# Kernel tuning notes

Hardware: AMD Instinct MI355X
Metric: run time of the kernel (lower is better)

The kernel has to match this reference:

```python
import jax, jax.numpy as jnp
import numpy as np


def _degree_norms(src, dst, n_nodes):
    ones = jnp.ones(src.shape[0], dtype=jnp.float32)
    deg_out = jax.ops.segment_sum(ones, src, num_segments=n_nodes)
    deg_in = jax.ops.segment_sum(ones, dst, num_segments=n_nodes)
    # DGL GraphConv clamps degrees to min 1 before pow(-0.5)
    norm_src = jnp.power(jnp.maximum(deg_out, 1.0), -0.5)
    norm_dst = jnp.power(jnp.maximum(deg_in, 1.0), -0.5)
    return norm_src, norm_dst


def _graph_conv(h, src, dst, norm_src, norm_dst, W, b, activation):
    n_nodes = h.shape[0]
    # norm='both': scale source features, project, aggregate, scale dest
    x = h * norm_src[:, None]
    x = x @ W                                   # [N, out]
    m = x[src]                                  # gather  [E, out]
    agg = jax.ops.segment_sum(m, dst, num_segments=n_nodes)  # scatter-add [N, out]
    out = agg * norm_dst[:, None] + b
    if activation is not None:
        out = activation(out)
    return out


def setup_inputs() -> dict:
    key = jax.random.key(0)
    k = jax.random.split(key, 6)
    N, E, F, D = 100000, 1600000, 128, 128
    feature = jax.random.normal(k[0], (N, F), dtype=jnp.float32)
    src = jax.random.randint(k[1], (E,), 0, N, dtype=jnp.int32)
    dst = jax.random.randint(k[2], (E,), 0, N, dtype=jnp.int32)
    W1 = jax.random.normal(k[3], (F, D), dtype=jnp.float32) / np.sqrt(F)
    b1 = jnp.zeros((D,), dtype=jnp.float32)
    W2 = jax.random.normal(k[4], (D, D), dtype=jnp.float32) / np.sqrt(D)
    b2 = jnp.zeros((D,), dtype=jnp.float32)
    return {"feature": feature, "src": src, "dst": dst,
            "W1": W1, "b1": b1, "W2": W2, "b2": b2}


def reference(feature, src, dst, W1, b1, W2, b2):
    n_nodes = feature.shape[0]
    norm_src, norm_dst = _degree_norms(src, dst, n_nodes)
    # layer 0: relu; layer 1 (last): no activation
    h = _graph_conv(feature, src, dst, norm_src, norm_dst, W1, b1, jax.nn.relu)
    h = _graph_conv(h, src, dst, norm_src, norm_dst, W2, b2, None)
    return h
```

## Files before the change

kernel.cpp:

```cpp
#include <hip/hip_runtime.h>


#define RS_LOG 10
#define RS (1 << RS_LOG)

__device__ __forceinline__ unsigned pack_bf2(float a, float b) {
  unsigned ua = __float_as_uint(a);
  ua = ua + 0x7FFF + ((ua >> 16) & 1);
  unsigned ub = __float_as_uint(b);
  ub = ub + 0x7FFF + ((ub >> 16) & 1);
  return (ua >> 16) | (ub & 0xFFFF0000u);
}

__global__ void build_graph(const int* __restrict__ src, const int* __restrict__ dst,
                            int* __restrict__ cursor, int* __restrict__ deg_out,
                            int* __restrict__ padded, int E, int CAP) {
  int e = blockIdx.x * blockDim.x + threadIdx.x;
  if (e < E) {
    int s = src[e];
    int d = dst[e];
    atomicAdd(&deg_out[s], 1);
    int pos = atomicAdd(&cursor[d], 1);
    if (pos < CAP) padded[(size_t)d * CAP + pos] = s;
  }
}

__global__ __launch_bounds__(256) void partition_edges(
    const int* __restrict__ src, const int* __restrict__ dst, int* __restrict__ g_cnt,
    int* __restrict__ part_dst, unsigned short* __restrict__ part_src, int E, int NR, int CAPR,
    int EPB) {
  __shared__ int cntD[256], cntS[256], baseD[256], baseS[256];
  int t = threadIdx.x;
  int e0 = blockIdx.x * EPB;
  int e1 = min(e0 + EPB, E);
  for (int i = t; i < NR; i += 256) {
    cntD[i] = 0;
    cntS[i] = 0;
  }
  __syncthreads();
  for (int e = e0 + t; e < e1; e += 256) {
    atomicAdd(&cntD[dst[e] >> RS_LOG], 1);
    atomicAdd(&cntS[src[e] >> RS_LOG], 1);
  }
  __syncthreads();
  for (int i = t; i < NR; i += 256) {
    baseD[i] = atomicAdd(&g_cnt[i * 16], cntD[i]);
    baseS[i] = atomicAdd(&g_cnt[(NR + i) * 16], cntS[i]);
    cntD[i] = 0;
    cntS[i] = 0;
  }
  __syncthreads();
  for (int e = e0 + t; e < e1; e += 256) {
    int s = src[e];
    int d = dst[e];
    int rd = d >> RS_LOG;
    int rs = s >> RS_LOG;
    int pd = baseD[rd] + atomicAdd(&cntD[rd], 1);
    if (pd < CAPR) part_dst[(size_t)rd * CAPR + pd] = ((d & (RS - 1)) << 17) | s;
    int ps = baseS[rs] + atomicAdd(&cntS[rs], 1);
    if (ps < CAPR) part_src[(size_t)rs * CAPR + ps] = (unsigned short)(s & (RS - 1));
  }
}

__global__ __launch_bounds__(512) void build_structures(
    const int* __restrict__ g_cnt, const int* __restrict__ part_dst,
    const unsigned short* __restrict__ part_src, int* __restrict__ padded,
    int* __restrict__ deg_in, int* __restrict__ deg_out, int N, int NR, int CAPR, int CAP) {
  __shared__ int cur[RS];
  int t = threadIdx.x;
  int b = blockIdx.x;
  for (int i = t; i < RS; i += 512) cur[i] = 0;
  __syncthreads();
  if (b < NR) {
    int cnt = min(g_cnt[b * 16], CAPR);
    const int* p = part_dst + (size_t)b * CAPR;
    for (int i = t; i < cnt; i += 512) {
      int v = p[i];
      int dlow = v >> 17;
      int s = v & 0x1FFFF;
      int pos = atomicAdd(&cur[dlow], 1);
      if (pos < CAP) padded[((size_t)((b << RS_LOG) + dlow)) * CAP + pos] = s;
    }
    __syncthreads();
    int nbase = b << RS_LOG;
    for (int i = t; i < RS; i += 512) {
      int node = nbase + i;
      if (node < N) deg_in[node] = cur[i];
    }
  } else {
    int r = b - NR;
    int cnt = min(g_cnt[(NR + r) * 16], CAPR);
    const unsigned short* p = part_src + (size_t)r * CAPR;
    for (int i = t; i < cnt; i += 512) atomicAdd(&cur[p[i]], 1);
    __syncthreads();
    int nbase = r << RS_LOG;
    for (int i = t; i < RS; i += 512) {
      int node = nbase + i;
      if (node < N) deg_out[node] = cur[i];
    }
  }
}

__global__ void compute_norms(const int* __restrict__ deg_out, const int* __restrict__ deg_in,
                              float* __restrict__ norm_src, float* __restrict__ norm_dst, int N) {
  int i = blockIdx.x * blockDim.x + threadIdx.x;
  if (i < N) {
    norm_src[i] = rsqrtf((float)max(deg_out[i], 1));
    norm_dst[i] = rsqrtf((float)max(deg_in[i], 1));
  }
}

__global__ __launch_bounds__(512) void gemm_scale_bf(const float* __restrict__ X,
                                                     const float* __restrict__ W,
                                                     const float* __restrict__ norm,
                                                     unsigned* __restrict__ Ybf, int N) {
  __shared__ float Xl[64 * 129];
  int t = threadIdx.x;
  int r0 = blockIdx.x * 64;
  {
    const float4* X4 = (const float4*)(X + (size_t)r0 * 128);
#pragma unroll
    for (int j = 0; j < 4; j++) {
      int idx4 = t + j * 512;
      int r = idx4 >> 5;
      int c4 = idx4 & 31;
      float4 v = {0.f, 0.f, 0.f, 0.f};
      if (r0 + r < N) v = X4[idx4];
      float* dp = &Xl[r * 129 + c4 * 4];
      dp[0] = v.x;
      dp[1] = v.y;
      dp[2] = v.z;
      dp[3] = v.w;
    }
  }
  __syncthreads();
  int lane = t & 63;
  int wv = t >> 6;
  int c0 = __builtin_amdgcn_readfirstlane(wv * 16);
  float acc[16];
#pragma unroll
  for (int u = 0; u < 16; u++) acc[u] = 0.f;
  const float* xrow = &Xl[lane * 129];
#pragma unroll 4
  for (int k = 0; k < 128; k++) {
    float xk = xrow[k];
    const float* wp = W + k * 128 + c0;
#pragma unroll
    for (int u = 0; u < 16; u++) acc[u] = fmaf(wp[u], xk, acc[u]);
  }
  int r = r0 + lane;
  if (r < N) {
    float nn = norm[r];
    unsigned p[8];
#pragma unroll
    for (int q = 0; q < 8; q++) p[q] = pack_bf2(acc[2 * q] * nn, acc[2 * q + 1] * nn);
    uint4* yo = (uint4*)(Ybf + (size_t)r * 64 + (c0 >> 1));
    yo[0] = make_uint4(p[0], p[1], p[2], p[3]);
    yo[1] = make_uint4(p[4], p[5], p[6], p[7]);
  }
}

__global__ __launch_bounds__(256) void spmm_bf(const unsigned* __restrict__ Ybf,
                                               const int* __restrict__ padded,
                                               const int* __restrict__ deg_in,
                                               const float* __restrict__ norm_dst,
                                               const float* __restrict__ bias,
                                               float* __restrict__ out, int N, int CAP,
                                               int do_relu) {
  int t = threadIdx.x;
  int lane = t & 63;
  int wv = t >> 6;
  int v = blockIdx.x * 4 + wv;
  if (v >= N) return;
  int cnt = min(deg_in[v], CAP);
  int sidx = (lane < cnt) ? padded[(size_t)v * CAP + lane] : 0;
  float ax = 0.f, ay = 0.f;
  int i = 0;
  for (; i + 4 <= cnt; i += 4) {
    int s0 = __builtin_amdgcn_readlane(sidx, i);
    int s1 = __builtin_amdgcn_readlane(sidx, i + 1);
    int s2 = __builtin_amdgcn_readlane(sidx, i + 2);
    int s3 = __builtin_amdgcn_readlane(sidx, i + 3);
    unsigned w0 = Ybf[(size_t)s0 * 64 + lane];
    unsigned w1 = Ybf[(size_t)s1 * 64 + lane];
    unsigned w2 = Ybf[(size_t)s2 * 64 + lane];
    unsigned w3 = Ybf[(size_t)s3 * 64 + lane];
    ax += __uint_as_float(w0 << 16) + __uint_as_float(w1 << 16) +
          __uint_as_float(w2 << 16) + __uint_as_float(w3 << 16);
    ay += __uint_as_float(w0 & 0xFFFF0000u) + __uint_as_float(w1 & 0xFFFF0000u) +
          __uint_as_float(w2 & 0xFFFF0000u) + __uint_as_float(w3 & 0xFFFF0000u);
  }
  for (; i < cnt; i++) {
    int s = __builtin_amdgcn_readlane(sidx, i);
    unsigned w = Ybf[(size_t)s * 64 + lane];
    ax += __uint_as_float(w << 16);
    ay += __uint_as_float(w & 0xFFFF0000u);
  }
  float nd = norm_dst[v];
  float2 b = ((const float2*)bias)[lane];
  float2 r;
  r.x = ax * nd + b.x;
  r.y = ay * nd + b.y;
  if (do_relu) {
    r.x = fmaxf(r.x, 0.f);
    r.y = fmaxf(r.y, 0.f);
  }
  ((float2*)out)[(size_t)v * 64 + lane] = r;
}

extern "C" void kernel_launch(void* const* d_in, const int* in_sizes, int n_in,
                              void* d_out, int out_size, void* d_ws, size_t ws_size,
                              hipStream_t stream) {
  const float* feature = (const float*)d_in[0];
  const int* src = (const int*)d_in[1];
  const int* dst = (const int*)d_in[2];
  const float* W1 = (const float*)d_in[3];
  const float* b1 = (const float*)d_in[4];
  const float* W2 = (const float*)d_in[5];
  const float* b2 = (const float*)d_in[6];
  float* out = (float*)d_out;

  const int F = 128;
  int N = in_sizes[0] / F;
  int E = in_sizes[1];
  (void)n_in;
  (void)out_size;

  char* ws = (char*)d_ws;
  size_t off = 0;
  auto alloc = [&](size_t bytes) -> char* {
    char* p = ws + off;
    off = (off + bytes + 255) & ~(size_t)255;
    return p;
  };
  float* h_buf = (float*)alloc((size_t)N * F * 4);
  int* degs = (int*)alloc((size_t)2 * N * 4);
  int* deg_in_ = degs;
  int* deg_out_ = degs + N;
  float* norm_src = (float*)alloc((size_t)N * 4);
  float* norm_dst = (float*)alloc((size_t)N * 4);

  int NR = (N + RS - 1) >> RS_LOG;
  int CAPR = (E + NR - 1) / NR + 4096;
  CAPR = (CAPR + 31) & ~31;
  size_t part_bytes =
      (size_t)NR * CAPR * 4 + (size_t)NR * CAPR * 2 + (size_t)2 * NR * 16 * 4 + 1024;
  size_t avail = (ws_size > off) ? ws_size - off : 0;

  int CAP;
  bool partition_ok = (N <= 131072) && (NR <= 256);
  bool use_part;
  if (partition_ok && avail >= (size_t)N * 64 * 4 + part_bytes) {
    CAP = 64;
    use_part = true;
  } else if (partition_ok && avail >= (size_t)N * 48 * 4 + part_bytes) {
    CAP = 48;
    use_part = true;
  } else if (avail >= (size_t)N * 64 * 4 + (size_t)N * 4 + 256) {
    CAP = 64;
    use_part = false;
  } else if (avail >= (size_t)N * 48 * 4 + (size_t)N * 4 + 256) {
    CAP = 48;
    use_part = false;
  } else {
    CAP = 32;
    use_part = false;
  }
  int* padded = (int*)alloc((size_t)N * CAP * 4);

  if (use_part) {
    int* part_dst = (int*)alloc((size_t)NR * CAPR * 4);
    unsigned short* part_src = (unsigned short*)alloc((size_t)NR * CAPR * 2);
    int* g_cnt = (int*)alloc((size_t)2 * NR * 16 * 4);
    const int EPB = 4096;
    int NB = (E + EPB - 1) / EPB;
    hipMemsetAsync(g_cnt, 0, (size_t)2 * NR * 16 * 4, stream);
    partition_edges<<<NB, 256, 0, stream>>>(src, dst, g_cnt, part_dst, part_src, E, NR, CAPR,
                                            EPB);
    build_structures<<<2 * NR, 512, 0, stream>>>(g_cnt, part_dst, part_src, padded, deg_in_,
                                                 deg_out_, N, NR, CAPR, CAP);
  } else {
    int* cursor = (int*)alloc((size_t)N * 4);
    hipMemsetAsync(degs, 0, (size_t)2 * N * 4, stream);
    build_graph<<<(E + 255) / 256, 256, 0, stream>>>(src, dst, deg_in_, deg_out_, padded, E, CAP);
    (void)cursor;
  }
  compute_norms<<<(N + 255) / 256, 256, 0, stream>>>(deg_out_, deg_in_, norm_src, norm_dst, N);

  unsigned* ybf1 = (unsigned*)d_out;
  unsigned* ybf2;
  float* final_target;
  bool need_copy;
  size_t ybf_bytes = (size_t)N * 64 * 4;
  if (ws_size > off && ws_size - off >= ybf_bytes + 256) {
    ybf2 = (unsigned*)alloc(ybf_bytes);
    final_target = out;
    need_copy = false;
  } else {
    ybf2 = (unsigned*)d_out;
    final_target = h_buf;
    need_copy = true;
  }

  int gblocks = (N + 63) / 64;
  gemm_scale_bf<<<gblocks, 512, 0, stream>>>(feature, W1, norm_src, ybf1, N);
  spmm_bf<<<(N + 3) / 4, 256, 0, stream>>>(ybf1, padded, deg_in_, norm_dst, b1, h_buf, N, CAP, 1);
  gemm_scale_bf<<<gblocks, 512, 0, stream>>>(h_buf, W2, norm_src, ybf2, N);
  spmm_bf<<<(N + 3) / 4, 256, 0, stream>>>(ybf2, padded, deg_in_, norm_dst, b2, final_target, N,
                                           CAP, 0);
  if (need_copy) {
    hipMemcpyAsync(out, h_buf, (size_t)N * F * 4, hipMemcpyDeviceToDevice, stream);
  }
}
```

Measured before the change: 400.4 us.

## Replace FP32 FMA GEMM with split-bf16 MFMA GEMM using pre-transposed weights

Replaces the scalar FP32 dense projection with a matrix-core kernel using 16x16x32 bf16 MFMA. Activations and weights are split into high and low bf16 parts, and three MFMA products are summed to approximate FP32 accuracy. A new prep kernel converts and transposes each weight matrix once per call. The change targets compute time in the two GEMMs, at the cost of extra conversion ALU work and uncoalesced 2-byte output stores.

Measured after the change: 414.1 us. +3.4%, slower.

```diff
diff --git a/kernel.cpp b/kernel.cpp
--- a/kernel.cpp
+++ b/kernel.cpp
@@ -4,12 +4,12 @@
 #define RS_LOG 10
 #define RS (1 << RS_LOG)
 
-__device__ __forceinline__ unsigned pack_bf2(float a, float b) {
-  unsigned ua = __float_as_uint(a);
-  ua = ua + 0x7FFF + ((ua >> 16) & 1);
-  unsigned ub = __float_as_uint(b);
-  ub = ub + 0x7FFF + ((ub >> 16) & 1);
-  return (ua >> 16) | (ub & 0xFFFF0000u);
+typedef short bf16x8 __attribute__((ext_vector_type(8)));
+typedef float f32x4 __attribute__((ext_vector_type(4)));
+
+__device__ __forceinline__ unsigned short rne_bf16(float v) {
+  unsigned u = __float_as_uint(v);
+  return (unsigned short)((u + 0x7FFF + ((u >> 16) & 1)) >> 16);
 }
 
 __global__ void build_graph(const int* __restrict__ src, const int* __restrict__ dst,
@@ -110,53 +110,98 @@
   }
 }
 
-__global__ __launch_bounds__(512) void gemm_scale_bf(const float* __restrict__ X,
-                                                     const float* __restrict__ W,
-                                                     const float* __restrict__ norm,
-                                                     unsigned* __restrict__ Ybf, int N) {
-  __shared__ float Xl[64 * 129];
+__global__ __launch_bounds__(256) void prep_w(const float* __restrict__ W,
+                                              unsigned short* __restrict__ Wt_hi,
+                                              unsigned short* __restrict__ Wt_lo) {
+  int idx = blockIdx.x * 256 + threadIdx.x;
+  int k = idx >> 7;
+  int c = idx & 127;
+  float w = W[idx];
+  unsigned short h = rne_bf16(w);
+  float hf = __uint_as_float((unsigned)h << 16);
+  unsigned short l = rne_bf16(w - hf);
+  Wt_hi[c * 128 + k] = h;
+  Wt_lo[c * 128 + k] = l;
+}
+
+__global__ __launch_bounds__(256) void gemm_mfma(const float* __restrict__ X,
+                                                 const unsigned short* __restrict__ Wt_hi,
+                                                 const unsigned short* __restrict__ Wt_lo,
+                                                 const float* __restrict__ norm,
+                                                 unsigned short* __restrict__ Ybf, int N) {
   int t = threadIdx.x;
-  int r0 = blockIdx.x * 64;
-  {
-    const float4* X4 = (const float4*)(X + (size_t)r0 * 128);
-#pragma unroll
-    for (int j = 0; j < 4; j++) {
-      int idx4 = t + j * 512;
-      int r = idx4 >> 5;
-      int c4 = idx4 & 31;
-      float4 v = {0.f, 0.f, 0.f, 0.f};
-      if (r0 + r < N) v = X4[idx4];
-      float* dp = &Xl[r * 129 + c4 * 4];
-      dp[0] = v.x;
-      dp[1] = v.y;
-      dp[2] = v.z;
-      dp[3] = v.w;
-    }
-  }
-  __syncthreads();
   int lane = t & 63;
   int wv = t >> 6;
-  int c0 = __builtin_amdgcn_readfirstlane(wv * 16);
-  float acc[16];
-#pragma unroll
-  for (int u = 0; u < 16; u++) acc[u] = 0.f;
-  const float* xrow = &Xl[lane * 129];
-#pragma unroll 4
-  for (int k = 0; k < 128; k++) {
-    float xk = xrow[k];
-    const float* wp = W + k * 128 + c0;
-#pragma unroll
-    for (int u = 0; u < 16; u++) acc[u] = fmaf(wp[u], xk, acc[u]);
-  }
-  int r = r0 + lane;
-  if (r < N) {
-    float nn = norm[r];
-    unsigned p[8];
-#pragma unroll
-    for (int q = 0; q < 8; q++) p[q] = pack_bf2(acc[2 * q] * nn, acc[2 * q + 1] * nn);
-    uint4* yo = (uint4*)(Ybf + (size_t)r * 64 + (c0 >> 1));
-    yo[0] = make_uint4(p[0], p[1], p[2], p[3]);
-    yo[1] = make_uint4(p[4], p[5], p[6], p[7]);
+  int r0 = blockIdx.x * 128;
+  int c = lane & 15;
+  int kgrp = lane >> 4;
+
+  int rowA0 = r0 + wv * 32 + c;
+  int rowA1 = rowA0 + 16;
+  bool ok0 = rowA0 < N;
+  bool ok1 = rowA1 < N;
+  float nn0 = ok0 ? norm[rowA0] : 0.f;
+  float nn1 = ok1 ? norm[rowA1] : 0.f;
+  const float* xr0 = X + (size_t)rowA0 * 128;
+  const float* xr1 = X + (size_t)rowA1 * 128;
+  const unsigned short* pbh = Wt_hi + (size_t)c * 128;
+  const unsigned short* pbl = Wt_lo + (size_t)c * 128;
+
+  f32x4 acc[2][8];
+#pragma unroll
+  for (int mr = 0; mr < 2; mr++)
+#pragma unroll
+    for (int nr = 0; nr < 8; nr++) acc[mr][nr] = (f32x4){0.f, 0.f, 0.f, 0.f};
+
+#pragma unroll
+  for (int s = 0; s < 4; s++) {
+    int kb = s * 32 + kgrp * 8;
+    bf16x8 ah[2], al[2];
+    {
+      float4 z = make_float4(0.f, 0.f, 0.f, 0.f);
+      float4 x0a = ok0 ? *(const float4*)(xr0 + kb) : z;
+      float4 x0b = ok0 ? *(const float4*)(xr0 + kb + 4) : z;
+      float4 x1a = ok1 ? *(const float4*)(xr1 + kb) : z;
+      float4 x1b = ok1 ? *(const float4*)(xr1 + kb + 4) : z;
+      float v0[8] = {x0a.x, x0a.y, x0a.z, x0a.w, x0b.x, x0b.y, x0b.z, x0b.w};
+      float v1[8] = {x1a.x, x1a.y, x1a.z, x1a.w, x1b.x, x1b.y, x1b.z, x1b.w};
+#pragma unroll
+      for (int j = 0; j < 8; j++) {
+        float a = v0[j] * nn0;
+        unsigned short h = rne_bf16(a);
+        ah[0][j] = (short)h;
+        al[0][j] = (short)rne_bf16(a - __uint_as_float((unsigned)h << 16));
+        float b = v1[j] * nn1;
+        unsigned short h2 = rne_bf16(b);
+        ah[1][j] = (short)h2;
+        al[1][j] = (short)rne_bf16(b - __uint_as_float((unsigned)h2 << 16));
+      }
+    }
+#pragma unroll
+    for (int nr = 0; nr < 8; nr++) {
+      bf16x8 bh = *(const bf16x8*)(pbh + nr * 2048 + kb);
+      bf16x8 bl = *(const bf16x8*)(pbl + nr * 2048 + kb);
+#pragma unroll
+      for (int mr = 0; mr < 2; mr++) {
+        acc[mr][nr] = __builtin_amdgcn_mfma_f32_16x16x32_bf16(ah[mr], bh, acc[mr][nr], 0, 0, 0);
+        acc[mr][nr] = __builtin_amdgcn_mfma_f32_16x16x32_bf16(al[mr], bh, acc[mr][nr], 0, 0, 0);
+        acc[mr][nr] = __builtin_amdgcn_mfma_f32_16x16x32_bf16(ah[mr], bl, acc[mr][nr], 0, 0, 0);
+      }
+    }
+  }
+
+#pragma unroll
+  for (int mr = 0; mr < 2; mr++) {
+    int rb = r0 + wv * 32 + mr * 16 + kgrp * 4;
+#pragma unroll
+    for (int q = 0; q < 4; q++) {
+      int row = rb + q;
+      if (row < N) {
+        unsigned short* yo = Ybf + (size_t)row * 128 + c;
+#pragma unroll
+        for (int nr = 0; nr < 8; nr++) yo[nr * 16] = rne_bf16(acc[mr][nr][q]);
+      }
+    }
   }
 }
 
@@ -239,6 +284,10 @@
   int* deg_out_ = degs + N;
   float* norm_src = (float*)alloc((size_t)N * 4);
   float* norm_dst = (float*)alloc((size_t)N * 4);
+  unsigned short* wt1_hi = (unsigned short*)alloc(128 * 128 * 2);
+  unsigned short* wt1_lo = (unsigned short*)alloc(128 * 128 * 2);
+  unsigned short* wt2_hi = (unsigned short*)alloc(128 * 128 * 2);
+  unsigned short* wt2_lo = (unsigned short*)alloc(128 * 128 * 2);
 
   int NR = (N + RS - 1) >> RS_LOG;
   int CAPR = (E + NR - 1) / NR + 4096;
@@ -268,6 +317,9 @@
   }
   int* padded = (int*)alloc((size_t)N * CAP * 4);
 
+  prep_w<<<64, 256, 0, stream>>>(W1, wt1_hi, wt1_lo);
+  prep_w<<<64, 256, 0, stream>>>(W2, wt2_hi, wt2_lo);
+
   if (use_part) {
     int* part_dst = (int*)alloc((size_t)NR * CAPR * 4);
     unsigned short* part_src = (unsigned short*)alloc((size_t)NR * CAPR * 2);
@@ -287,27 +339,28 @@
   }
   compute_norms<<<(N + 255) / 256, 256, 0, stream>>>(deg_out_, deg_in_, norm_src, norm_dst, N);
 
-  unsigned* ybf1 = (unsigned*)d_out;
-  unsigned* ybf2;
+  unsigned short* ybf1 = (unsigned short*)d_out;
+  unsigned short* ybf2;
   float* final_target;
   bool need_copy;
-  size_t ybf_bytes = (size_t)N * 64 * 4;
+  size_t ybf_bytes = (size_t)N * 128 * 2;
   if (ws_size > off && ws_size - off >= ybf_bytes + 256) {
-    ybf2 = (unsigned*)alloc(ybf_bytes);
+    ybf2 = (unsigned short*)alloc(ybf_bytes);
     final_target = out;
     need_copy = false;
   } else {
-    ybf2 = (unsigned*)d_out;
+    ybf2 = (unsigned short*)d_out;
     final_target = h_buf;
     need_copy = true;
   }
 
-  int gblocks = (N + 63) / 64;
-  gemm_scale_bf<<<gblocks, 512, 0, stream>>>(feature, W1, norm_src, ybf1, N);
-  spmm_bf<<<(N + 3) / 4, 256, 0, stream>>>(ybf1, padded, deg_in_, norm_dst, b1, h_buf, N, CAP, 1);
-  gemm_scale_bf<<<gblocks, 512, 0, stream>>>(h_buf, W2, norm_src, ybf2, N);
-  spmm_bf<<<(N + 3) / 4, 256, 0, stream>>>(ybf2, padded, deg_in_, norm_dst, b2, final_target, N,
-                                           CAP, 0);
+  int gblocks = (N + 127) / 128;
+  gemm_mfma<<<gblocks, 256, 0, stream>>>(feature, wt1_hi, wt1_lo, norm_src, ybf1, N);
+  spmm_bf<<<(N + 3) / 4, 256, 0, stream>>>((const unsigned*)ybf1, padded, deg_in_, norm_dst, b1,
+                                           h_buf, N, CAP, 1);
+  gemm_mfma<<<gblocks, 256, 0, stream>>>(h_buf, wt2_hi, wt2_lo, norm_src, ybf2, N);
+  spmm_bf<<<(N + 3) / 4, 256, 0, stream>>>((const unsigned*)ybf2, padded, deg_in_, norm_dst, b2,
+                                           final_target, N, CAP, 0);
   if (need_copy) {
     hipMemcpyAsync(out, h_buf, (size_t)N * F * 4, hipMemcpyDeviceToDevice, stream);
   }
```
